# Kernel tuning notes

Measured on AMD Instinct MI355X. Metric: run time of the kernel, lower is better.

## Reference

```python
import jax, jax.numpy as jnp
import numpy as np

B, C, H, W = 8, 256, 128, 128
S = C // 4          # squeezed channels (squeeze_factor=4)
HEADS = 8

def _conv(x, w, pad, groups=1):
    # NCHW conv, stride 1
    return jax.lax.conv_general_dilated(
        x, w, (1, 1), [(pad, pad), (pad, pad)],
        feature_group_count=groups,
        dimension_numbers=('NCHW', 'OIHW', 'NCHW'))

def _cln(x, w, b):
    # WithBias LayerNorm over channel dim (to_3d -> LN over c -> to_4d)
    mu = jnp.mean(x, axis=1, keepdims=True)
    var = jnp.mean((x - mu) ** 2, axis=1, keepdims=True)
    return (x - mu) * jax.lax.rsqrt(var + 1e-5) * w[None, :, None, None] + b[None, :, None, None]

def setup_inputs() -> dict:
    key = jax.random.key(0)
    ks = jax.random.split(key, 14)
    r = lambda i, shape, s=0.05: jax.random.normal(ks[i], shape, jnp.float32) * s
    return dict(
        x=r(0, (B, C, H, W), 1.0),
        y=r(1, (B, C, H, W), 1.0),
        w_cq=r(2, (S, C, 3, 3)),          # compress_q
        w_ckv=r(3, (S, C, 3, 3)),         # compress_kv
        ln_q_w=jnp.ones(S), ln_q_b=jnp.zeros(S),
        ln_kv_w=jnp.ones(S), ln_kv_b=jnp.zeros(S),
        w_kv=r(4, (2 * S, S, 1, 1)),      # kv 1x1
        w_kvdw=r(5, (2 * S, 1, 3, 3)),    # kv depthwise 3x3
        w_q=r(6, (S, S, 3, 3)),           # q 3x3
        temperature=jnp.ones((HEADS, 1, 1)),
        w_po=r(7, (S, S, 1, 1)),          # project_out 1x1
        w_expand=r(8, (C, S, 3, 3)),      # expand 3x3
        ln_out_w=jnp.ones(C), ln_out_b=jnp.zeros(C),
        w_ffn1=r(9, (C, 2 * C, 1, 1)),    # ffn conv1x1 (dim_q+dim_kv -> dim_out)
        w_ffn_dw=r(10, (C, 1, 3, 3)),     # ffn depthwise 3x3
        w_ffn2=r(11, (C, C, 1, 1)),       # ffn conv1x1
    )

def reference(x, y, w_cq, w_ckv, ln_q_w, ln_q_b, ln_kv_w, ln_kv_b,
              w_kv, w_kvdw, w_q, temperature, w_po, w_expand,
              ln_out_w, ln_out_b, w_ffn1, w_ffn_dw, w_ffn2):
    # channel compress + LayerNorm
    xq = _cln(_conv(x, w_cq, 1), ln_q_w, ln_q_b)      # [B,S,H,W]
    ykv = _cln(_conv(y, w_ckv, 1), ln_kv_w, ln_kv_b)  # [B,S,H,W]
    b, c, h, w = xq.shape
    # cross channel attention
    kv = _conv(_conv(ykv, w_kv, 0), w_kvdw, 1, groups=2 * c)
    k, v = jnp.split(kv, 2, axis=1)
    q = _conv(xq, w_q, 1)
    sh = lambda t: t.reshape(b, HEADS, c // HEADS, h * w)  # b head c (hw)
    q, k, v = sh(q), sh(k), sh(v)
    q = q / jnp.maximum(jnp.linalg.norm(q, axis=-1, keepdims=True), 1e-12)
    k = k / jnp.maximum(jnp.linalg.norm(k, axis=-1, keepdims=True), 1e-12)
    attn = jax.nn.softmax(
        jnp.einsum('bhcn,bhdn->bhcd', q, k) * temperature[None], axis=-1)
    o = jnp.einsum('bhcd,bhdn->bhcn', attn, v).reshape(b, c, h, w)
    o = _conv(o, w_po, 0)
    # expand back to full channels, norm, conv FFN
    vexp = _conv(o, w_expand, 1)                      # [B,C,H,W]
    vn = _cln(vexp, ln_out_w, ln_out_b)
    cat = jnp.concatenate([x, vn], axis=1)            # [B,2C,H,W]
    f = _conv(cat, w_ffn1, 0)
    f = jax.nn.gelu(_conv(f, w_ffn_dw, 1, groups=f.shape[1]), approximate=False)
    return _conv(f, w_ffn2, 0)
```

## Files before the change

### kernel.cpp

```cpp
#include <hip/hip_runtime.h>
#include <hip/hip_bf16.h>
#include <math.h>

#define B_ 8
#define C_ 256
#define S_ 64
#define H_ 128
#define W_ 128
#define HW_ (H_*W_)
#define P_ (B_*HW_)

typedef __attribute__((ext_vector_type(8))) short short8;
typedef __attribute__((ext_vector_type(4))) float f32x4;

__device__ __forceinline__ unsigned short f2b(float f){
    __hip_bfloat16 h = __float2bfloat16(f);
    return *reinterpret_cast<unsigned short*>(&h);
}
__device__ __forceinline__ void up8(uint4 u, float* f){
    unsigned v0=u.x,v1=u.y,v2=u.z,v3=u.w;
    f[0]=__uint_as_float(v0<<16); f[1]=__uint_as_float(v0&0xffff0000u);
    f[2]=__uint_as_float(v1<<16); f[3]=__uint_as_float(v1&0xffff0000u);
    f[4]=__uint_as_float(v2<<16); f[5]=__uint_as_float(v2&0xffff0000u);
    f[6]=__uint_as_float(v3<<16); f[7]=__uint_as_float(v3&0xffff0000u);
}
__device__ __forceinline__ uint4 pk8(const float* f){
    uint4 u;
    u.x = (unsigned)f2b(f[0]) | ((unsigned)f2b(f[1])<<16);
    u.y = (unsigned)f2b(f[2]) | ((unsigned)f2b(f[3])<<16);
    u.z = (unsigned)f2b(f[4]) | ((unsigned)f2b(f[5])<<16);
    u.w = (unsigned)f2b(f[6]) | ((unsigned)f2b(f[7])<<16);
    return u;
}
__device__ __forceinline__ void gl2lds(const unsigned short* g, unsigned short* l){
    __builtin_amdgcn_global_load_lds((const __attribute__((address_space(1))) void*)g,
                                     (__attribute__((address_space(3))) void*)l, 16, 0, 0);
}


__global__ __launch_bounds__(256) void pack_k(const float* __restrict__ inA,
                                              const float* __restrict__ inB,
                                              unsigned short* __restrict__ outA,
                                              unsigned short* __restrict__ outB)
{
    __shared__ unsigned short tl[64][72];
    const int t = threadIdx.x;
    const int p0 = blockIdx.x*64, c0 = blockIdx.y*64;
    const int sel = blockIdx.z >> 3, b = blockIdx.z & 7;
    const float* in = sel ? inB : inA;
    unsigned short* out = sel ? outB : outA;
    const float* ib = in + ((size_t)b*C_ + c0)*HW_ + p0;
    for (int i = t; i < 1024; i += 256){
        int ci = i >> 4, px = (i & 15)*4;
        float4 v = *(const float4*)(ib + (size_t)ci*HW_ + px);
        tl[px+0][ci]=f2b(v.x); tl[px+1][ci]=f2b(v.y); tl[px+2][ci]=f2b(v.z); tl[px+3][ci]=f2b(v.w);
    }
    __syncthreads();
    for (int i = t; i < 512; i += 256){
        int px = i >> 3, c8 = (i & 7)*8;
        int cc = c0 + c8;
        unsigned short* dst = out + ((size_t)b*8 + (cc>>5))*(size_t)HW_*32
                                  + (size_t)(p0+px)*32 + (cc&31);
        *(uint4*)dst = *(uint4*)&tl[px][c8];
    }
}

__device__ __forceinline__ void packw(const float* __restrict__ src, unsigned short* __restrict__ dst,
                                      int e, int CO, int CI, int KS2)
{
    int KB = CI/32;
    int tap = e / (CO*CI);
    int rem = e % (CO*CI);
    int coT = rem / (CI*16);
    int rem2 = rem % (CI*16);
    int kb = rem2 >> 9;
    int l  = (rem2 >> 3) & 63;
    int ee = rem2 & 7;
    int co = coT*16 + (l & 15);
    int ci = kb*32 + (l >> 4)*8 + ee;
    float v = (KS2==9) ? src[(size_t)(co*CI+ci)*9 + tap] : src[(size_t)co*CI + ci];
    dst[e] = f2b(v);
}

__global__ __launch_bounds__(256) void prep_k(const float* __restrict__ cq, const float* __restrict__ ckv,
                                              const float* __restrict__ q,  const float* __restrict__ kv,
                                              const float* __restrict__ f1, const float* __restrict__ f2,
                                              const float* __restrict__ dwk, const float* __restrict__ dwf,
                                              unsigned short* o_cq, unsigned short* o_ckv, unsigned short* o_q,
                                              unsigned short* o_kv, unsigned short* o_f1, unsigned short* o_f2,
                                              unsigned short* o_dwk, unsigned short* o_dwf)
{
    int i = blockIdx.x*256 + threadIdx.x;
    if      (i < 147456) packw(cq,  o_cq,  i,          64, 256, 9);
    else if (i < 294912) packw(ckv, o_ckv, i-147456,   64, 256, 9);
    else if (i < 331776) packw(q,   o_q,   i-294912,   64,  64, 9);
    else if (i < 339968) packw(kv,  o_kv,  i-331776,  128,  64, 1);
    else if (i < 471040) packw(f1,  o_f1,  i-339968,  256, 512, 1);
    else if (i < 536576) packw(f2,  o_f2,  i-471040,  256, 256, 1);
    else if (i < 537728) { int e=i-536576; o_dwk[e] = f2b(dwk[(e&127)*9 + (e>>7)]); }
    else if (i < 540032) { int e=i-537728; o_dwf[e] = f2b(dwf[(e&255)*9 + (e>>8)]); }
    else if (i < 540040) { o_dwf[i-537728] = 0; }
}

template<int C0,int C1,int COUT,int KS,int OUTM,int LNF>
__global__ __launch_bounds__(256,4) void mconv_k(
    const unsigned short* __restrict__ in0, int s0,
    const unsigned short* __restrict__ in1, int s1,
    const unsigned short* __restrict__ wp, long wpbs,
    void* __restrict__ outp, int so,
    const unsigned short* __restrict__ in0B,
    const unsigned short* __restrict__ wpB2,
    void* __restrict__ outB,
    const unsigned short* __restrict__ zbuf,
    const float* __restrict__ lnw0, const float* __restrict__ lnb0,
    const float* __restrict__ lnw1, const float* __restrict__ lnb1,
    int ny, int nz)
{
    constexpr int CINT = C0+C1;
    constexpr int KB  = CINT/32;
    constexpr int MT  = 4;
    constexpr int NT  = 2;
    constexpr int RWS = (KS==3)?4:1;
    constexpr int PXS = (KS==3)?66:128;
    constexpr int NTR = RWS*PXS*4;
    constexpr int NLD = (NTR+255)/256;
    constexpr int ASZ = RWS*PXS*32;
    constexpr int EP  = (OUTM==1) ? 64*132*2 : 128*64;
    constexpr int SSZ = (2*ASZ > EP) ? 2*ASZ : EP;
    __shared__ alignas(16) unsigned short sbuf[SSZ];

    const int t = threadIdx.x;
    const int nper = (128*ny*nz) >> 3;
    int lin = (blockIdx.x & 7)*nper + (blockIdx.x >> 3);
    const int gy_ = lin % ny;
    int rem = lin / ny;
    const int gx_ = rem & 127;
    const int gz_ = rem >> 7;
    const int sel = gz_ >> 3;
    const int b   = gz_ & 7;
    const int cob = gy_*64;

    const unsigned short* pin0 = sel ? in0B : in0;
    const unsigned short* wpb  = (sel ? wpB2 : wp) + (size_t)b*wpbs;

    int y0=0,x0=0; size_t p0=0;
    if (KS==3){ y0=(gx_>>1)*2; x0=(gx_&1)*64; }
    else p0 = (size_t)gx_*128;

    const int l = t&63, w = t>>6;
    const int wy = w>>1, wx = w&1;
    const int lrow = l&15, lk = l>>4;

    const size_t b0base = (size_t)b*HW_*s0;
    const size_t b1base = (size_t)b*HW_*s1;

    auto issueA = [&](int kb, int bsel){
        const int cg = kb*32;
        unsigned short* dst = sbuf + bsel*ASZ;
        #pragma unroll
        for (int j=0;j<NLD;++j){
            int i = t + j*256;
            if ((NTR%256)==0 || j<NLD-1 || i<NTR){
                int slot = i&3, pr = i>>2;
                int px = pr%PXS, row = pr/PXS;
                int g = slot ^ (px&3);
                int c = cg + g*8;
                const unsigned short* sp;
                if (KS==3){
                    int gy = y0+row-1, gx = x0+px-1;
                    bool ok = ((unsigned)gy<(unsigned)H_) & ((unsigned)gx<(unsigned)W_);
                    size_t p = (size_t)gy*W_+gx;
                    const unsigned short* base = (c<C0)
                        ? pin0 + b0base + ((size_t)(c>>5)*HW_ + p)*32 + (c&31)
                        : in1  + b1base + ((size_t)((c-C0)>>5)*HW_ + p)*32 + ((c-C0)&31);
                    sp = ok ? base : zbuf;
                } else {
                    size_t p = p0+px;
                    sp = (c<C0)
                        ? pin0 + b0base + ((size_t)(c>>5)*HW_ + p)*32 + (c&31)
                        : in1  + b1base + ((size_t)((c-C0)>>5)*HW_ + p)*32 + ((c-C0)&31);
                }
                gl2lds(sp, dst + (size_t)i*8);
            }
        }
    };
    auto loadB = [&](short8* dst, int kb, int tap){
        #pragma unroll
        for (int n=0;n<NT;++n){
            int fi = (tap*(COUT/16) + (cob>>4) + wx*NT + n)*KB + kb;
            dst[n] = *(const short8*)(wpb + (size_t)fi*512 + l*8);
        }
    };

    f32x4 acc[MT][NT] = {};

    if (KS==3){
        short8 bfs[3][NT];
        issueA(0,0);
        loadB(bfs[0],0,0); loadB(bfs[1],0,1); loadB(bfs[2],0,2);
        for (int kb=0; kb<KB; ++kb){
            __syncthreads();
            unsigned short* cur = sbuf + (kb&1)*ASZ;
            #pragma unroll
            for (int tap=0;tap<9;++tap){
                const int ky=tap/3, kx=tap%3;
                if (tap==2 && kb+1<KB) issueA(kb+1,(kb+1)&1);
                short8 af[MT];
                #pragma unroll
                for (int m=0;m<MT;++m){
                    int pl = wy*64 + m*16 + lrow;
                    int r = (pl>>6)+ky, xx = (pl&63)+kx;
                    af[m] = *(const short8*)&cur[((r*PXS+xx)*4 + (lk^(xx&3)))*8];
                }
                #pragma unroll
                for (int m=0;m<MT;++m)
                    #pragma unroll
                    for (int n=0;n<NT;++n)
                        acc[m][n] = __builtin_amdgcn_mfma_f32_16x16x32_bf16(af[m],bfs[tap%3][n],acc[m][n],0,0,0);
                if (tap+3 < 9)      loadB(bfs[tap%3], kb, tap+3);
                else if (kb+1<KB)   loadB(bfs[tap%3], kb+1, tap-6);
            }
        }
    } else {
        short8 bfs[2][NT];
        issueA(0,0);
        loadB(bfs[0],0,0); if (KB>1) loadB(bfs[1],1,0);
        auto step1 = [&](int kb, short8 (&bcur)[NT]){
            __syncthreads();
            unsigned short* cur = sbuf + (kb&1)*ASZ;
            if (kb+1<KB) issueA(kb+1,(kb+1)&1);
            short8 af[MT];
            #pragma unroll
            for (int m=0;m<MT;++m){
                int pl = wy*64 + m*16 + lrow;
                af[m] = *(const short8*)&cur[(pl*4 + (lk^(pl&3)))*8];
            }
            #pragma unroll
            for (int m=0;m<MT;++m)
                #pragma unroll
                for (int n=0;n<NT;++n)
                    acc[m][n] = __builtin_amdgcn_mfma_f32_16x16x32_bf16(af[m],bcur[n],acc[m][n],0,0,0);
            if (kb+2<KB) loadB(bcur, kb+2, 0);
        };
        for (int kb2=0; kb2<KB; kb2+=2){
            step1(kb2,   bfs[0]);
            step1(kb2+1, bfs[1]);
        }
    }
    __syncthreads();

    if (OUTM==1){
        float* sf = (float*)sbuf;
        #pragma unroll
        for (int m=0;m<MT;++m)
            #pragma unroll
            for (int n=0;n<NT;++n){
                int co_l = wx*32 + n*16 + lrow;
                int pl0  = wy*64 + m*16 + lk*4;
                *(f32x4*)&sf[co_l*132 + pl0] = acc[m][n];
            }
        __syncthreads();
        float* out = (float*)(sel ? outB : outp);
        for (int i=t; i<2048; i+=256){
            int co = i>>5, pxg = i&31;
            f32x4 v = *(const f32x4*)&sf[co*132 + pxg*4];
            *(f32x4*)(out + ((size_t)(b*COUT + cob + co))*HW_ + p0 + pxg*4) = v;
        }
    } else if (LNF){
        #pragma unroll
        for (int m=0;m<MT;++m)
            #pragma unroll
            for (int n=0;n<NT;++n){
                int co = wx*32 + n*16 + lrow;
                int grp = co>>3, cr = co&7;
                #pragma unroll
                for (int r=0;r<4;++r){
                    int pl = wy*64 + m*16 + lk*4 + r;
                    sbuf[pl*64 + ((grp^(pl&7))<<3) + cr] = f2b(acc[m][n][r]);
                }
            }
        __syncthreads();
        if (t < 128){
            int pl = t;
            uint4 raw[8];
            float s = 0.f, ss = 0.f;
            #pragma unroll
            for (int j=0;j<8;++j){
                raw[j] = *(const uint4*)&sbuf[pl*64 + ((j^(pl&7))<<3)];
                float f[8]; up8(raw[j], f);
                #pragma unroll
                for (int k=0;k<8;++k){ s += f[k]; ss += f[k]*f[k]; }
            }
            float mu = s*(1.f/64.f);
            float rs = rsqrtf(ss*(1.f/64.f) - mu*mu + 1e-5f);
            const float* lw = sel ? lnw1 : lnw0;
            const float* lb = sel ? lnb1 : lnb0;
            unsigned short* out = (unsigned short*)(sel ? outB : outp);
            size_t p = (size_t)(y0+(pl>>6))*W_ + x0 + (pl&63);
            #pragma unroll
            for (int j=0;j<8;++j){
                float f[8], o[8];
                up8(raw[j], f);
                #pragma unroll
                for (int k=0;k<8;++k) o[k] = (f[k]-mu)*rs*lw[j*8+k] + lb[j*8+k];
                int cc = j*8;
                unsigned short* dst = out + ((size_t)b*2 + (cc>>5))*(size_t)HW_*32 + p*32 + (cc&31);
                *(uint4*)dst = pk8(o);
            }
        }
    } else {
        unsigned short* out = (unsigned short*)(sel ? outB : outp);
        #pragma unroll
        for (int m=0;m<MT;++m)
            #pragma unroll
            for (int n=0;n<NT;++n){
                int co = wx*32 + n*16 + lrow;
                #pragma unroll
                for (int r=0;r<4;++r){
                    int pl = wy*64 + m*16 + lk*4 + r;
                    sbuf[pl*64 + co] = f2b(acc[m][n][r]);
                }
            }
        __syncthreads();
        for (int i=t; i<1024; i+=256){
            int pl = i>>3, c8 = (i&7)*8;
            size_t p = (KS==3) ? ((size_t)(y0+(pl>>6))*W_ + (size_t)(x0+(pl&63))) : (p0+pl);
            int cc = cob + c8;
            unsigned short* dst = out + (size_t)b*HW_*so + ((size_t)(cc>>5)*HW_ + p)*32 + (cc&31);
            *(uint4*)dst = *(uint4*)&sbuf[pl*64 + c8];
        }
    }
}

template<int C>
__global__ __launch_bounds__(256) void cln_k(unsigned short* __restrict__ io,
                                             const float* __restrict__ wg,
                                             const float* __restrict__ bi)
{
    constexpr int L = C/8;
    size_t idx = (size_t)blockIdx.x*256 + threadIdx.x;
    int sub = (int)(idx % L);
    size_t pix = idx / L;
    int b = (int)(pix >> 14);
    size_t p = pix & (HW_-1);
    unsigned short* rp = io + ((size_t)b*(C/32) + (sub>>2))*(size_t)HW_*32 + p*32 + (sub&3)*8;
    uint4 raw = *(const uint4*)rp;
    float f[8]; up8(raw, f);
    float s = 0.f, ss = 0.f;
    #pragma unroll
    for (int j=0;j<8;++j){ s += f[j]; ss += f[j]*f[j]; }
    #pragma unroll
    for (int m=1;m<L;m<<=1){ s += __shfl_xor(s,m); ss += __shfl_xor(ss,m); }
    float mu = s*(1.f/C);
    float rs = rsqrtf(ss*(1.f/C) - mu*mu + 1e-5f);
    float4 w0 = *(const float4*)(wg+sub*8), w1 = *(const float4*)(wg+sub*8+4);
    float4 b0 = *(const float4*)(bi+sub*8), b1 = *(const float4*)(bi+sub*8+4);
    float o[8];
    o[0]=(f[0]-mu)*rs*w0.x+b0.x; o[1]=(f[1]-mu)*rs*w0.y+b0.y;
    o[2]=(f[2]-mu)*rs*w0.z+b0.z; o[3]=(f[3]-mu)*rs*w0.w+b0.w;
    o[4]=(f[4]-mu)*rs*w1.x+b1.x; o[5]=(f[5]-mu)*rs*w1.y+b1.y;
    o[6]=(f[6]-mu)*rs*w1.z+b1.z; o[7]=(f[7]-mu)*rs*w1.w+b1.w;
    *(uint4*)rp = pk8(o);
}

template<int CH, bool GELU>
__global__ __launch_bounds__(256) void dw_k(const unsigned short* __restrict__ in,
                                            const unsigned short* __restrict__ wp,
                                            unsigned short* __restrict__ out)
{
    size_t idx = (size_t)blockIdx.x*256 + threadIdx.x;
    int c8 = (int)(idx % (CH/8));
    size_t pix = idx / (CH/8);
    int p = (int)(pix % HW_);
    int b = (int)(pix / HW_);
    int yy = p >> 7, xx = p & 127;
    const unsigned short* ib = in + ((size_t)b*(CH/32) + (c8>>2))*(size_t)HW_*32 + (c8&3)*8;
    float wf[9][8];
    #pragma unroll
    for (int tap=0; tap<9; ++tap){
        uint4 r = *(const uint4*)(wp + tap*CH + c8*8);
        up8(r, wf[tap]);
    }
    float a[8] = {0,0,0,0,0,0,0,0};
    #pragma unroll
    for (int ky=0; ky<3; ++ky){
        int gy = yy+ky-1;
        if ((unsigned)gy >= (unsigned)H_) continue;
        #pragma unroll
        for (int kx=0; kx<3; ++kx){
            int gx = xx+kx-1;
            if ((unsigned)gx >= (unsigned)W_) continue;
            uint4 r = *(const uint4*)(ib + (size_t)(gy*W_+gx)*32);
            float f[8]; up8(r, f);
            #pragma unroll
            for (int j=0;j<8;++j) a[j] += f[j]*wf[ky*3+kx][j];
        }
    }
    if (GELU){
        #pragma unroll
        for (int j=0;j<8;++j) a[j] = 0.5f*a[j]*(1.f + erff(a[j]*0.70710678118654752f));
    }
    unsigned short* ob = out + ((size_t)b*(CH/32) + (c8>>2))*(size_t)HW_*32 + (size_t)p*32 + (c8&3)*8;
    *(uint4*)ob = pk8(a);
}

__global__ __launch_bounds__(256) void attn_k(const unsigned short* __restrict__ qc,
                                              const unsigned short* __restrict__ kvd,
                                              const float* __restrict__ temp,
                                              float* __restrict__ probs)
{
    int b = blockIdx.x >> 3, h = blockIdx.x & 7;
    int t = threadIdx.x;
    const unsigned short* qb = qc  + ((size_t)b*2 + (h>>2))*(size_t)HW_*32 + (h&3)*8;
    const unsigned short* kb = kvd + ((size_t)b*4 + (h>>2))*(size_t)HW_*32 + (h&3)*8;
    float qs[8] = {}, ks[8] = {}, dt[8][8] = {{}};
    for (int p = t; p < HW_; p += 256){
        float qv[8], kv[8];
        up8(*(const uint4*)(qb + (size_t)p*32), qv);
        up8(*(const uint4*)(kb + (size_t)p*32), kv);
        #pragma unroll
        for (int i=0;i<8;++i){ qs[i]+=qv[i]*qv[i]; ks[i]+=kv[i]*kv[i]; }
        #pragma unroll
        for (int i=0;i<8;++i)
            #pragma unroll
            for (int j=0;j<8;++j) dt[i][j] += qv[i]*kv[j];
    }
    __shared__ float red[4][80];
    __shared__ float fin[80];
    int lane = t & 63, wv = t >> 6;
    #pragma unroll
    for (int i=0;i<8;++i){ float v=qs[i]; for (int m=1;m<64;m<<=1) v += __shfl_xor(v,m); if(!lane) red[wv][i]=v; }
    #pragma unroll
    for (int i=0;i<8;++i){ float v=ks[i]; for (int m=1;m<64;m<<=1) v += __shfl_xor(v,m); if(!lane) red[wv][8+i]=v; }
    #pragma unroll
    for (int i=0;i<8;++i)
        #pragma unroll
        for (int j=0;j<8;++j){ float v=dt[i][j]; for (int m=1;m<64;m<<=1) v += __shfl_xor(v,m); if(!lane) red[wv][16+i*8+j]=v; }
    __syncthreads();
    if (t < 80) fin[t] = red[0][t]+red[1][t]+red[2][t]+red[3][t];
    __syncthreads();
    if (t < 8){
        int i = t;
        float qn = fmaxf(sqrtf(fin[i]), 1e-12f);
        float tm = temp[h];
        float lg[8]; float mx = -1e30f;
        #pragma unroll
        for (int j=0;j<8;++j){
            float kn = fmaxf(sqrtf(fin[8+j]), 1e-12f);
            lg[j] = fin[16+i*8+j]/(qn*kn)*tm;
            mx = fmaxf(mx, lg[j]);
        }
        float se = 0.f;
        #pragma unroll
        for (int j=0;j<8;++j){ lg[j]=expf(lg[j]-mx); se+=lg[j]; }
        float inv = 1.f/se;
        #pragma unroll
        for (int j=0;j<8;++j) probs[(((size_t)b*8+h)*8+i)*8+j] = lg[j]*inv;
    }
}

__global__ __launch_bounds__(256) void mb_k(const float* __restrict__ probs,
                                            const float* __restrict__ wpo,
                                            float* __restrict__ Mb)
{
    int b = blockIdx.x;
    for (int o = threadIdx.x; o < 4096; o += 256){
        int co = o >> 6, d = o & 63, h = d >> 3, j = d & 7;
        float s = 0.f;
        #pragma unroll
        for (int i2=0;i2<8;++i2)
            s += wpo[co*64 + h*8 + i2] * probs[(((size_t)b*8+h)*8+i2)*8 + j];
        Mb[(size_t)b*4096 + o] = s;
    }
}

__global__ __launch_bounds__(256) void weff_k(const float* __restrict__ Mb,
                                              const float* __restrict__ wex,
                                              unsigned short* __restrict__ weff)
{
    int b = blockIdx.x / 576;
    int i = (blockIdx.x % 576)*256 + threadIdx.x;
    int tap = i / 16384;
    int rem = i % 16384;
    int coT = rem / 1024;
    int rem2 = rem % 1024;
    int kb = rem2 >> 9;
    int l  = (rem2 >> 3) & 63;
    int ee = rem2 & 7;
    int eo = coT*16 + (l & 15);
    int d  = kb*32 + (l >> 4)*8 + ee;
    const float* mb = Mb + (size_t)b*4096;
    float s = 0.f;
    #pragma unroll 8
    for (int c=0;c<64;++c)
        s += wex[(size_t)(eo*64+c)*9 + tap] * mb[c*64 + d];
    weff[(size_t)b*147456 + i] = f2b(s);
}

extern "C" void kernel_launch(void* const* d_in, const int* in_sizes, int n_in,
                              void* d_out, int out_size, void* d_ws, size_t ws_size,
                              hipStream_t stream) {
    (void)in_sizes; (void)n_in; (void)out_size; (void)ws_size;
    const float* x        = (const float*)d_in[0];
    const float* y        = (const float*)d_in[1];
    const float* w_cq     = (const float*)d_in[2];
    const float* w_ckv    = (const float*)d_in[3];
    const float* ln_q_w   = (const float*)d_in[4];
    const float* ln_q_b   = (const float*)d_in[5];
    const float* ln_kv_w  = (const float*)d_in[6];
    const float* ln_kv_b  = (const float*)d_in[7];
    const float* w_kv     = (const float*)d_in[8];
    const float* w_kvdw   = (const float*)d_in[9];
    const float* w_q      = (const float*)d_in[10];
    const float* temperature = (const float*)d_in[11];
    const float* w_po     = (const float*)d_in[12];
    const float* w_expand = (const float*)d_in[13];
    const float* ln_out_w = (const float*)d_in[14];
    const float* ln_out_b = (const float*)d_in[15];
    const float* w_ffn1   = (const float*)d_in[16];
    const float* w_ffn_dw = (const float*)d_in[17];
    const float* w_ffn2   = (const float*)d_in[18];
    float* outp = (float*)d_out;

    const size_t MB = 1u<<20;
    char* ws8 = (char*)d_ws;
    unsigned short* ykv  = (unsigned short*)(ws8 + 0);
    unsigned short* xq   = (unsigned short*)(ws8 + 16*MB);
    unsigned short* kv1  = (unsigned short*)(ws8 + 32*MB);
    unsigned short* qc   = (unsigned short*)(ws8 + 64*MB);
    unsigned short* kvd  = (unsigned short*)(ws8 + 80*MB);
    unsigned short* vexp = (unsigned short*)(ws8 + 0);
    unsigned short* f2b_ = (unsigned short*)(ws8 + 0);
    float* probs = (float*)(ws8 + 112*MB);
    float* Mb    = (float*)(ws8 + 113*MB);
    unsigned short* weff = (unsigned short*)(ws8 + 114*MB);
    unsigned short* wpB  = (unsigned short*)(ws8 + 117*MB);
    unsigned short* wp_cq  = wpB;
    unsigned short* wp_ckv = wpB + 147456;
    unsigned short* wp_q   = wpB + 294912;
    unsigned short* wp_kv  = wpB + 331776;
    unsigned short* wp_f1  = wpB + 339968;
    unsigned short* wp_f2  = wpB + 471040;
    unsigned short* wp_dwk = wpB + 536576;
    unsigned short* wp_dwf = wpB + 537728;
    unsigned short* zbuf   = wpB + 540032;
    unsigned short* xb = (unsigned short*)d_out;
    unsigned short* yb = (unsigned short*)d_out + 32*MB;
    unsigned short* f1 = yb;

    const unsigned short* NUL = (const unsigned short*)nullptr;

    prep_k<<<2111, 256, 0, stream>>>(w_cq, w_ckv, w_q, w_kv, w_ffn1, w_ffn2, w_kvdw, w_ffn_dw,
                                     wp_cq, wp_ckv, wp_q, wp_kv, wp_f1, wp_f2, wp_dwk, wp_dwf);
    pack_k<<<dim3(256,4,16), 256, 0, stream>>>(y, x, yb, xb);
    mconv_k<256,0,64,3,0,1><<<128*1*16, 256, 0, stream>>>(yb,256, NUL,0, wp_ckv,0, ykv,64,
        xb, wp_cq, xq, zbuf, ln_kv_w, ln_kv_b, ln_q_w, ln_q_b, 1, 16);
    mconv_k<64,0,128,1,0,0><<<128*2*8, 256, 0, stream>>>(ykv,64, NUL,0, wp_kv,0, kv1,128,
        ykv, wp_kv, kv1, zbuf, NULL,NULL,NULL,NULL, 2, 8);
    mconv_k<64,0,64,3,0,0><<<128*1*8, 256, 0, stream>>>(xq,64, NUL,0, wp_q,0, qc,64,
        xq, wp_q, qc, zbuf, NULL,NULL,NULL,NULL, 1, 8);
    dw_k<128,false><<<8192, 256, 0, stream>>>(kv1, wp_dwk, kvd);
    attn_k<<<64, 256, 0, stream>>>(qc, kvd, temperature, probs);
    mb_k<<<8, 256, 0, stream>>>(probs, w_po, Mb);
    weff_k<<<4608, 256, 0, stream>>>(Mb, w_expand, weff);
    mconv_k<64,0,256,3,0,0><<<128*4*8, 256, 0, stream>>>(kvd + (size_t)HW_*64,128, NUL,0, weff,147456, vexp,256,
        kvd + (size_t)HW_*64, weff, vexp, zbuf, NULL,NULL,NULL,NULL, 4, 8);
    cln_k<256><<<16384, 256, 0, stream>>>(vexp, ln_out_w, ln_out_b);
    mconv_k<256,256,256,1,0,0><<<128*4*8, 256, 0, stream>>>(xb,256, vexp,256, wp_f1,0, f1,256,
        xb, wp_f1, f1, zbuf, NULL,NULL,NULL,NULL, 4, 8);
    dw_k<256,true><<<16384, 256, 0, stream>>>(f1, wp_dwf, f2b_);
    mconv_k<256,0,256,1,1,0><<<128*4*8, 256, 0, stream>>>(f2b_,256, NUL,0, wp_f2,0, outp,0,
        f2b_, wp_f2, outp, zbuf, NULL,NULL,NULL,NULL, 4, 8);
}
```

Baseline: 578.1 us.

## Double K-chunk per stage in 1x1 conv, widen LDS swizzle, prefetch earlier

For the 1x1 conv path, each pipeline stage now stages two 32-channel K blocks (64 channels) into LDS, which halves the number of barriers per K loop. The LDS swizzle XOR now also mixes in bits 2-3 of the pixel index, meant to cut bank conflicts on the fragment reads. For the 3x3 path, the next-stage global-to-LDS prefetch is issued right after the barrier rather than at tap 2. The 1x1 path now assumes KB is even and at least 2, and its LDS footprint grows.

Result: faster. 519.3 us (-10.2%).

```diff
diff --git a/kernel.cpp b/kernel.cpp
--- a/kernel.cpp
+++ b/kernel.cpp
@@ -120,11 +120,8 @@
     constexpr int KB  = CINT/32;
     constexpr int MT  = 4;
     constexpr int NT  = 2;
-    constexpr int RWS = (KS==3)?4:1;
     constexpr int PXS = (KS==3)?66:128;
-    constexpr int NTR = RWS*PXS*4;
-    constexpr int NLD = (NTR+255)/256;
-    constexpr int ASZ = RWS*PXS*32;
+    constexpr int ASZ = (KS==3)? 4*66*32 : 8192;
     constexpr int EP  = (OUTM==1) ? 64*132*2 : 128*64;
     constexpr int SSZ = (2*ASZ > EP) ? 2*ASZ : EP;
     __shared__ alignas(16) unsigned short sbuf[SSZ];
@@ -154,33 +151,43 @@
     const size_t b0base = (size_t)b*HW_*s0;
     const size_t b1base = (size_t)b*HW_*s1;
 
-    auto issueA = [&](int kb, int bsel){
+    auto issueA3 = [&](int kb, int bsel){
         const int cg = kb*32;
         unsigned short* dst = sbuf + bsel*ASZ;
         #pragma unroll
-        for (int j=0;j<NLD;++j){
+        for (int j=0;j<5;++j){
             int i = t + j*256;
-            if ((NTR%256)==0 || j<NLD-1 || i<NTR){
+            if (j<4 || i<1056){
                 int slot = i&3, pr = i>>2;
-                int px = pr%PXS, row = pr/PXS;
-                int g = slot ^ (px&3);
+                int px = pr%66, row = pr/66;
+                int g = slot ^ (px&3) ^ ((px>>2)&3);
                 int c = cg + g*8;
-                const unsigned short* sp;
-                if (KS==3){
-                    int gy = y0+row-1, gx = x0+px-1;
-                    bool ok = ((unsigned)gy<(unsigned)H_) & ((unsigned)gx<(unsigned)W_);
-                    size_t p = (size_t)gy*W_+gx;
-                    const unsigned short* base = (c<C0)
-                        ? pin0 + b0base + ((size_t)(c>>5)*HW_ + p)*32 + (c&31)
-                        : in1  + b1base + ((size_t)((c-C0)>>5)*HW_ + p)*32 + ((c-C0)&31);
-                    sp = ok ? base : zbuf;
-                } else {
-                    size_t p = p0+px;
-                    sp = (c<C0)
-                        ? pin0 + b0base + ((size_t)(c>>5)*HW_ + p)*32 + (c&31)
-                        : in1  + b1base + ((size_t)((c-C0)>>5)*HW_ + p)*32 + ((c-C0)&31);
-                }
-                gl2lds(sp, dst + (size_t)i*8);
+                int gy = y0+row-1, gx = x0+px-1;
+                bool ok = ((unsigned)gy<(unsigned)H_) & ((unsigned)gx<(unsigned)W_);
+                size_t p = (size_t)gy*W_+gx;
+                const unsigned short* base = (c<C0)
+                    ? pin0 + b0base + ((size_t)(c>>5)*HW_ + p)*32 + (c&31)
+                    : in1  + b1base + ((size_t)((c-C0)>>5)*HW_ + p)*32 + ((c-C0)&31);
+                gl2lds(ok ? base : zbuf, dst + (size_t)i*8);
+            }
+        }
+    };
+    auto issueA1 = [&](int s, int bsel){
+        unsigned short* dst = sbuf + bsel*ASZ;
+        #pragma unroll
+        for (int h=0;h<2;++h){
+            const int cg = (s*2+h)*32;
+            #pragma unroll
+            for (int j=0;j<2;++j){
+                int i = t + j*256;
+                int slot = i&3, px = i>>2;
+                int g = slot ^ (px&3) ^ ((px>>2)&3);
+                int c = cg + g*8;
+                size_t p = p0+px;
+                const unsigned short* sp = (c<C0)
+                    ? pin0 + b0base + ((size_t)(c>>5)*HW_ + p)*32 + (c&31)
+                    : in1  + b1base + ((size_t)((c-C0)>>5)*HW_ + p)*32 + ((c-C0)&31);
+                gl2lds(sp, dst + (size_t)(h*4096 + i*8));
             }
         }
     };
@@ -196,21 +203,21 @@
 
     if (KS==3){
         short8 bfs[3][NT];
-        issueA(0,0);
+        issueA3(0,0);
         loadB(bfs[0],0,0); loadB(bfs[1],0,1); loadB(bfs[2],0,2);
         for (int kb=0; kb<KB; ++kb){
             __syncthreads();
+            if (kb+1<KB) issueA3(kb+1,(kb+1)&1);
             unsigned short* cur = sbuf + (kb&1)*ASZ;
             #pragma unroll
             for (int tap=0;tap<9;++tap){
                 const int ky=tap/3, kx=tap%3;
-                if (tap==2 && kb+1<KB) issueA(kb+1,(kb+1)&1);
                 short8 af[MT];
                 #pragma unroll
                 for (int m=0;m<MT;++m){
                     int pl = wy*64 + m*16 + lrow;
                     int r = (pl>>6)+ky, xx = (pl&63)+kx;
-                    af[m] = *(const short8*)&cur[((r*PXS+xx)*4 + (lk^(xx&3)))*8];
+                    af[m] = *(const short8*)&cur[((r*PXS+xx)*4 + (lk^(xx&3)^((xx>>2)&3)))*8];
                 }
                 #pragma unroll
                 for (int m=0;m<MT;++m)
@@ -222,29 +229,29 @@
             }
         }
     } else {
+        constexpr int KBS = (KB>=2) ? KB/2 : 1;
         short8 bfs[2][NT];
-        issueA(0,0);
-        loadB(bfs[0],0,0); if (KB>1) loadB(bfs[1],1,0);
-        auto step1 = [&](int kb, short8 (&bcur)[NT]){
+        issueA1(0,0);
+        loadB(bfs[0],0,0); loadB(bfs[1],1,0);
+        for (int s=0; s<KBS; ++s){
             __syncthreads();
-            unsigned short* cur = sbuf + (kb&1)*ASZ;
-            if (kb+1<KB) issueA(kb+1,(kb+1)&1);
-            short8 af[MT];
-            #pragma unroll
-            for (int m=0;m<MT;++m){
-                int pl = wy*64 + m*16 + lrow;
-                af[m] = *(const short8*)&cur[(pl*4 + (lk^(pl&3)))*8];
-            }
-            #pragma unroll
-            for (int m=0;m<MT;++m)
-                #pragma unroll
-                for (int n=0;n<NT;++n)
-                    acc[m][n] = __builtin_amdgcn_mfma_f32_16x16x32_bf16(af[m],bcur[n],acc[m][n],0,0,0);
-            if (kb+2<KB) loadB(bcur, kb+2, 0);
-        };
-        for (int kb2=0; kb2<KB; kb2+=2){
-            step1(kb2,   bfs[0]);
-            step1(kb2+1, bfs[1]);
+            if (s+1<KBS) issueA1(s+1,(s+1)&1);
+            unsigned short* cur = sbuf + (s&1)*ASZ;
+            #pragma unroll
+            for (int j=0;j<2;++j){
+                short8 af[MT];
+                #pragma unroll
+                for (int m=0;m<MT;++m){
+                    int pl = wy*64 + m*16 + lrow;
+                    af[m] = *(const short8*)&cur[j*4096 + (pl*4 + (lk^(pl&3)^((pl>>2)&3)))*8];
+                }
+                #pragma unroll
+                for (int m=0;m<MT;++m)
+                    #pragma unroll
+                    for (int n=0;n<NT;++n)
+                        acc[m][n] = __builtin_amdgcn_mfma_f32_16x16x32_bf16(af[m],bfs[j][n],acc[m][n],0,0,0);
+                if (s*2+j+2 < KB) loadB(bfs[j], s*2+j+2, 0);
+            }
         }
     }
     __syncthreads();
```
